# Optimization experiments

Hardware: AMD Instinct MI355X
Metric: run time of the kernel (lower is better)

Reference implementation:

```python
import jax, jax.numpy as jnp
import numpy as np

N_LAYER, N_HEAD, N_EMBD, VOCAB, T_CTX, MAXT, B = 6, 8, 128, 18, 30, 2719, 64


def _ln(x, g, b, eps=1e-5):
    m = x.mean(-1, keepdims=True)
    v = ((x - m) ** 2).mean(-1, keepdims=True)
    return (x - m) * jax.lax.rsqrt(v + eps) * g + b


def setup_inputs() -> dict:
    key = jax.random.key(0)
    ks = iter(jax.random.split(key, 64))
    nrm = lambda shape: jax.random.normal(next(ks), shape, jnp.float32) * 0.02
    E, L4 = N_EMBD, 4 * N_EMBD
    inp = dict(
        states=jax.random.normal(next(ks), (B, T_CTX, 4, 84, 84), jnp.float32),
        actions=jax.random.randint(next(ks), (B, T_CTX, 1), 0, VOCAB),
        rtgs=jax.random.normal(next(ks), (B, T_CTX, 1), jnp.float32),
        timesteps=jax.random.randint(next(ks), (B, 1, 1), 0, MAXT),
        conv_w=nrm((E, 4, 84, 84)),
        class_tok=nrm((1, 1, E)),
        in_proj_w=nrm((3 * E, E)), in_proj_b=jnp.zeros(3 * E),
        out_w=nrm((E, E)), out_b=jnp.zeros(E),
        iln1_g=jnp.ones(E), iln1_b=jnp.zeros(E),
        iln2_g=jnp.ones(E), iln2_b=jnp.zeros(E),
        ffn_w1=nrm((E, E)), ffn_b1=jnp.zeros(E),
        ffn_w2=nrm((E, E)), ffn_b2=jnp.zeros(E),
        ret_w=nrm((E, 1)), ret_b=jnp.zeros(E),
        act_table=nrm((VOCAB, E)),
        pos_emb=nrm((1, 3 * T_CTX + 1, E)),
        global_pos_emb=nrm((1, MAXT + 1, E)),
        ln1_g=jnp.ones((N_LAYER, E)), ln1_b=jnp.zeros((N_LAYER, E)),
        Wq=nrm((N_LAYER, E, E)), bq=jnp.zeros((N_LAYER, E)),
        Wk=nrm((N_LAYER, E, E)), bk=jnp.zeros((N_LAYER, E)),
        Wv=nrm((N_LAYER, E, E)), bv=jnp.zeros((N_LAYER, E)),
        Wo=nrm((N_LAYER, E, E)), bo=jnp.zeros((N_LAYER, E)),
        ln2_g=jnp.ones((N_LAYER, E)), ln2_b=jnp.zeros((N_LAYER, E)),
        W1=nrm((N_LAYER, L4, E)), b1=jnp.zeros((N_LAYER, L4)),
        W2=nrm((N_LAYER, E, L4)), b2=jnp.zeros((N_LAYER, E)),
        lnf_g=jnp.ones(E), lnf_b=jnp.zeros(E),
        head_w=nrm((VOCAB, E)),
    )
    return inp


def _forward(states, actions, rtgs, timesteps, conv_w, class_tok, in_proj_w, in_proj_b,
             out_w, out_b, iln1_g, iln1_b, iln2_g, iln2_b, ffn_w1, ffn_b1, ffn_w2, ffn_b2,
             ret_w, ret_b, act_table, pos_emb, global_pos_emb,
             ln1_g, ln1_b, Wq, bq, Wk, bk, Wv, bv, Wo, bo, ln2_g, ln2_b,
             W1, b1, W2, b2, lnf_g, lnf_b, head_w):
    Bsz, T = states.shape[:2]
    E = conv_w.shape[0]
    H, hd = N_HEAD, E // N_HEAD
    # --- inner TIT: patch embed (kernel 84 = frame size -> single patch = one big dot) ---
    obs = states.reshape(Bsz * T, *states.shape[2:])                      # (BT,4,84,84)
    patch = jnp.einsum('bchw,echw->be', obs, conv_w)[:, None, :]          # (BT,1,E)
    x = jnp.concatenate([jnp.broadcast_to(class_tok, (Bsz * T, 1, E)), patch], axis=1)  # (BT,2,E)
    h = _ln(x, iln1_g, iln1_b)
    q, k, v = jnp.split(h @ in_proj_w.T + in_proj_b, 3, axis=-1)
    att = jax.nn.softmax(jnp.einsum('bqe,bke->bqk', q, k) / jnp.sqrt(jnp.float32(E)), axis=-1)
    x = x + jnp.einsum('bqk,bke->bqe', att, v) @ out_w.T + out_b
    h2 = _ln(x, iln2_g, iln2_b)
    x = x + jax.nn.relu(h2 @ ffn_w1.T + ffn_b1) @ ffn_w2.T + ffn_b2
    state_emb = x[:, 0, :].reshape(Bsz, T, E)                             # class token
    # --- token interleave (targets=None path -> length 3T-1, last T-1 actions) ---
    rtg_emb = jnp.tanh(rtgs @ ret_w.T + ret_b)                            # (B,T,E)
    act_emb = jnp.tanh(act_table[actions[..., 0]])                        # (B,T,E)
    Lt = 3 * T - 1
    tok = jnp.zeros((Bsz, Lt, E), states.dtype)
    tok = tok.at[:, 0::3].set(rtg_emb).at[:, 1::3].set(state_emb).at[:, 2::3].set(act_emb[:, 1:])
    pos = global_pos_emb[0][timesteps[:, 0, 0]][:, None, :] + pos_emb[:, :Lt, :]
    x = tok + pos
    # --- outer causal GPT blocks ---
    mask = jnp.tril(jnp.ones((Lt, Lt), bool))
    for i in range(N_LAYER):
        hh = _ln(x, ln1_g[i], ln1_b[i])
        proj = lambda w, b: (hh @ w.T + b).reshape(Bsz, Lt, H, hd).transpose(0, 2, 1, 3)
        q, k, v = proj(Wq[i], bq[i]), proj(Wk[i], bk[i]), proj(Wv[i], bv[i])
        att = jnp.einsum('bhqd,bhkd->bhqk', q, k) / jnp.sqrt(jnp.float32(hd))
        att = jax.nn.softmax(jnp.where(mask, att, -jnp.inf), axis=-1)
        y = jnp.einsum('bhqk,bhkd->bhqd', att, v).transpose(0, 2, 1, 3).reshape(Bsz, Lt, E)
        x = x + y @ Wo[i].T + bo[i]
        hh2 = _ln(x, ln2_g[i], ln2_b[i])
        x = x + jax.nn.gelu(hh2 @ W1[i].T + b1[i], approximate=False) @ W2[i].T + b2[i]
    logits = _ln(x, lnf_g, lnf_b) @ head_w.T
    return logits[:, 1::3, :]                                             # (B,T,vocab) state-position logits


def reference(states, actions, rtgs, timesteps, conv_w, class_tok, in_proj_w, in_proj_b,
              out_w, out_b, iln1_g, iln1_b, iln2_g, iln2_b, ffn_w1, ffn_b1, ffn_w2, ffn_b2,
              ret_w, ret_b, act_table, pos_emb, global_pos_emb,
              ln1_g, ln1_b, Wq, bq, Wk, bk, Wv, bv, Wo, bo, ln2_g, ln2_b,
              W1, b1, W2, b2, lnf_g, lnf_b, head_w):
    return _forward(states, actions, rtgs, timesteps, conv_w, class_tok, in_proj_w, in_proj_b,
                    out_w, out_b, iln1_g, iln1_b, iln2_g, iln2_b, ffn_w1, ffn_b1, ffn_w2, ffn_b2,
                    ret_w, ret_b, act_table, pos_emb, global_pos_emb,
                    ln1_g, ln1_b, Wq, bq, Wk, bk, Wv, bv, Wo, bo, ln2_g, ln2_b,
                    W1, b1, W2, b2, lnf_g, lnf_b, head_w)
```

## Files before the change

### kernel.cpp

```cpp
#include <hip/hip_runtime.h>

#define NB   64
#define NT   30
#define NBT  1920
#define EE   128
#define KP   28224
#define LTK  89
#define NS   5696
#define NLY  6
#define NV   18
#define NZ   21

typedef unsigned short ushort_t;
using bf16x8 = __attribute__((ext_vector_type(8))) short;
using us8    = __attribute__((ext_vector_type(8))) unsigned short;
using f32x4  = __attribute__((ext_vector_type(4))) float;
using f32x16 = __attribute__((ext_vector_type(16))) float;

__device__ inline ushort_t f2bf(float f){
  union { float f; unsigned u; } v; v.f = f;
  unsigned r = v.u + 0x7FFFu + ((v.u >> 16) & 1u);
  return (ushort_t)(r >> 16);
}

__global__ __launch_bounds__(256) void wcvt(
  const float* conv, const float* Wq, const float* Wk, const float* Wv,
  const float* Wo, const float* W1, const float* W2,
  const float* in_w, const float* out_w, const float* f1w, const float* f2w,
  const float* bq, const float* bk, const float* bv,
  ushort_t* dc, ushort_t* dqkv, ushort_t* dout, ushort_t* d1, ushort_t* d2,
  ushort_t* dinw, ushort_t* doutw, ushort_t* df1, ushort_t* df2, float* bqkv)
{
  if (blockIdx.x >= 4776){
    int idx = (blockIdx.x-4776)*256 + threadIdx.x;
    if (idx < NLY*128){ int l=idx>>7, j=idx&127;
      bqkv[l*384+j]=bq[idx]; bqkv[l*384+128+j]=bk[idx]; bqkv[l*384+256+j]=bv[idx]; }
    return;
  }
  long i = 4l*((long)blockIdx.x*256 + threadIdx.x);
  if (i >= 3612672l && i < 3907584l){
    long o = i - 3612672l;
    int  seg = (int)(o / 98304l);
    long off2 = o - (long)seg*98304l;
    long layer = off2 >> 14, rem = off2 & 16383l;
    const float* s = (seg==0) ? Wq : (seg==1) ? Wk : Wv;
    float4 f = *reinterpret_cast<const float4*>(s+off2);
    long dst = layer*49152l + (long)seg*16384l + rem;
    dqkv[dst]=f2bf(f.x); dqkv[dst+1]=f2bf(f.y); dqkv[dst+2]=f2bf(f.z); dqkv[dst+3]=f2bf(f.w);
    return;
  }
  const float* s; ushort_t* d; long off;
  if      (i < 3612672l){ s=conv;  d=dc;    off=i; }
  else if (i < 4005888l){ s=Wo;    d=dout;  off=i-3907584l; }
  else if (i < 4399104l){ s=W1;    d=d1;    off=i-4005888l; }
  else if (i < 4792320l){ s=W2;    d=d2;    off=i-4399104l; }
  else if (i < 4841472l){ s=in_w;  d=dinw;  off=i-4792320l; }
  else if (i < 4857856l){ s=out_w; d=doutw; off=i-4841472l; }
  else if (i < 4874240l){ s=f1w;   d=df1;   off=i-4857856l; }
  else                  { s=f2w;   d=df2;   off=i-4874240l; }
  float4 f = *reinterpret_cast<const float4*>(s+off);
  d[off]=f2bf(f.x); d[off+1]=f2bf(f.y); d[off+2]=f2bf(f.z); d[off+3]=f2bf(f.w);
}

__global__ __launch_bounds__(256) void patch_gemm(
  const float* __restrict__ A, const ushort_t* __restrict__ Wb, float* __restrict__ C)
{
  __shared__ __align__(16) ushort_t As[64*64];
  __shared__ __align__(16) ushort_t Ws[128*64];
  const int tid = threadIdx.x, lane = tid & 63, wid = tid >> 6;
  const int m0 = blockIdx.x * 64;
  const int kbase = blockIdx.z * 1344;
  float* Cz = C + (size_t)blockIdx.z * NBT * EE;
  const int ra = tid>>2, ca = (tid&3)*16, swa = (ra&7)<<3;
  const int rw = tid>>1, cw = (tid&1)*32, sww = (rw&7)<<3;
  const float*    Ab = A  + (size_t)(m0+ra)*KP + kbase + ca;
  const ushort_t* Wp = Wb + (size_t)rw*KP  + kbase + cw;
  f32x4 acc[8];
  #pragma unroll
  for (int j=0;j<8;j++) acc[j] = (f32x4){0.f,0.f,0.f,0.f};
  float4 fa[4]; us8 wr[4];
  #pragma unroll
  for (int q=0;q<4;q++) fa[q] = *reinterpret_cast<const float4*>(Ab + 4*q);
  #pragma unroll
  for (int q=0;q<4;q++) wr[q] = *reinterpret_cast<const us8*>(Wp + 8*q);

  for (int kt = 0; kt < 21; ++kt){
    { us8 o0, o1;
      o0[0]=f2bf(fa[0].x); o0[1]=f2bf(fa[0].y); o0[2]=f2bf(fa[0].z); o0[3]=f2bf(fa[0].w);
      o0[4]=f2bf(fa[1].x); o0[5]=f2bf(fa[1].y); o0[6]=f2bf(fa[1].z); o0[7]=f2bf(fa[1].w);
      o1[0]=f2bf(fa[2].x); o1[1]=f2bf(fa[2].y); o1[2]=f2bf(fa[2].z); o1[3]=f2bf(fa[2].w);
      o1[4]=f2bf(fa[3].x); o1[5]=f2bf(fa[3].y); o1[6]=f2bf(fa[3].z); o1[7]=f2bf(fa[3].w);
      *reinterpret_cast<us8*>(&As[ra*64 + ( ca    ^ swa)]) = o0;
      *reinterpret_cast<us8*>(&As[ra*64 + ((ca+8) ^ swa)]) = o1;
      #pragma unroll
      for (int q=0;q<4;q++)
        *reinterpret_cast<us8*>(&Ws[rw*64 + ((cw+8*q) ^ sww)]) = wr[q];
    }
    if (kt < 20){
      #pragma unroll
      for (int q=0;q<4;q++) fa[q] = *reinterpret_cast<const float4*>(Ab + (kt+1)*64 + 4*q);
      #pragma unroll
      for (int q=0;q<4;q++) wr[q] = *reinterpret_cast<const us8*>(Wp + (kt+1)*64 + 8*q);
    }
    __syncthreads();
    #pragma unroll
    for (int ks=0; ks<2; ++ks){
      int arow = wid*16 + (lane&15);
      int kb = ks*32 + (lane>>4)*8;
      bf16x8 a = *reinterpret_cast<const bf16x8*>(&As[arow*64 + (kb ^ ((arow&7)<<3))]);
      #pragma unroll
      for (int nt=0; nt<8; ++nt){
        int nn = nt*16 + (lane&15);
        bf16x8 b = *reinterpret_cast<const bf16x8*>(&Ws[nn*64 + (kb ^ ((nn&7)<<3))]);
        acc[nt] = __builtin_amdgcn_mfma_f32_16x16x32_bf16(a, b, acc[nt], 0,0,0);
      }
    }
    __syncthreads();
  }
  #pragma unroll
  for (int nt=0; nt<8; ++nt)
    #pragma unroll
    for (int rr=0;rr<4;rr++){
      int row = m0 + wid*16 + (lane>>4)*4 + rr;
      int col = nt*16 + (lane&15);
      Cz[row*EE + col] = acc[nt][rr];
    }
}

__global__ __launch_bounds__(256, 1) void inner_tit(
  const float* __restrict__ part, const float* __restrict__ ctok,
  const ushort_t* __restrict__ inw, const float* __restrict__ in_b,
  const ushort_t* __restrict__ outw, const float* __restrict__ out_b,
  const float* __restrict__ g1, const float* __restrict__ b1_,
  const float* __restrict__ g2, const float* __restrict__ b2_,
  const ushort_t* __restrict__ f1wb, const float* __restrict__ fb1,
  const ushort_t* __restrict__ f2wb, const float* __restrict__ fb2,
  const float* __restrict__ rtgs, const int* __restrict__ actions,
  const int* __restrict__ tsteps, const float* __restrict__ ret_w,
  const float* __restrict__ ret_b, const float* __restrict__ act_tab,
  const float* __restrict__ pos_emb, const float* __restrict__ gpos,
  const float* __restrict__ ln1g0, const float* __restrict__ ln1b0,
  float* __restrict__ x, ushort_t* __restrict__ xln)
{
  __shared__ __align__(16) ushort_t wbuf[384*128];
  __shared__ float xs[16*128];
  __shared__ __align__(16) ushort_t hb[16*128];
  __shared__ __align__(16) ushort_t hf[16*128];
  __shared__ float qkv[16*384];
  __shared__ float ssm[32];
  const int tid = threadIdx.x, lane = tid & 63, wid = tid >> 6;
  const int bt0 = blockIdx.x * 8;

  auto stageWB = [&](const ushort_t* src, int R, int rowoff){
    for (int c = tid; c < R*16; c += 256){
      int rr = c >> 4, cc = (c & 15) * 8;
      *reinterpret_cast<us8*>(&wbuf[(rowoff+rr)*128 + (cc ^ ((rr&7)<<3))]) =
        *reinterpret_cast<const us8*>(src + (size_t)rr*128 + cc);
    }
  };
  auto lnrow = [&](const float* gam, const float* bet, ushort_t* dst){
    int r = tid >> 4, e0 = (tid & 15) * 8;
    float v[8];
    #pragma unroll
    for (int j=0;j<8;j++) v[j] = xs[r*128 + e0 + j];
    float s = 0;
    #pragma unroll
    for (int j=0;j<8;j++) s += v[j];
    s += __shfl_xor(s,1); s += __shfl_xor(s,2); s += __shfl_xor(s,4); s += __shfl_xor(s,8);
    float mean = s * (1.0f/128.0f);
    float vs = 0;
    #pragma unroll
    for (int j=0;j<8;j++){ float d = v[j]-mean; vs += d*d; }
    vs += __shfl_xor(vs,1); vs += __shfl_xor(vs,2); vs += __shfl_xor(vs,4); vs += __shfl_xor(vs,8);
    float rstd = rsqrtf(vs*(1.0f/128.0f) + 1e-5f);
    us8 o;
    #pragma unroll
    for (int j=0;j<8;j++) o[j] = f2bf((v[j]-mean)*rstd*gam[e0+j] + bet[e0+j]);
    *reinterpret_cast<us8*>(&dst[r*128 + (e0 ^ ((r&7)<<3))]) = o;
  };

  { int r = tid >> 4, e0 = (tid & 15) * 8;
    float v[8];
    if ((r & 1) == 0){
      #pragma unroll
      for (int j=0;j<8;j++) v[j] = ctok[e0+j];
    } else {
      #pragma unroll
      for (int j=0;j<8;j++) v[j] = 0.f;
      int bt = bt0 + (r>>1);
      for (int z=0; z<NZ; ++z){
        const float* p = part + (size_t)z*NBT*EE + (size_t)bt*128 + e0;
        float4 f0 = *reinterpret_cast<const float4*>(p);
        float4 f1 = *reinterpret_cast<const float4*>(p+4);
        v[0]+=f0.x; v[1]+=f0.y; v[2]+=f0.z; v[3]+=f0.w;
        v[4]+=f1.x; v[5]+=f1.y; v[6]+=f1.z; v[7]+=f1.w;
      }
    }
    #pragma unroll
    for (int j=0;j<8;j++) xs[r*128 + e0 + j] = v[j];
  }
  stageWB(inw, 384, 0);
  __syncthreads();

  lnrow(g1, b1_, hb);
  __syncthreads();

  { int al = lane & 15, kq = (lane>>4)*8;
    #pragma unroll
    for (int j=0;j<6;++j){
      int nt = wid*6 + j;
      f32x4 acc = (f32x4){0.f,0.f,0.f,0.f};
      int nrow = nt*16 + al, nsw = (nrow&7)<<3;
      #pragma unroll
      for (int ks=0; ks<4; ++ks){
        int kb = ks*32 + kq;
        bf16x8 a = *reinterpret_cast<const bf16x8*>(&hb[al*128 + (kb ^ ((al&7)<<3))]);
        bf16x8 b = *reinterpret_cast<const bf16x8*>(&wbuf[nrow*128 + (kb ^ nsw)]);
        acc = __builtin_amdgcn_mfma_f32_16x16x32_bf16(a, b, acc, 0,0,0);
      }
      float bia = in_b[nt*16 + al];
      #pragma unroll
      for (int rr=0; rr<4; ++rr){
        int row = (lane>>4)*4 + rr;
        qkv[row*384 + nt*16 + al] = acc[rr] + bia;
      }
    }
  }
  __syncthreads();

  { int d = tid >> 3, j = tid & 7;
    int i = d >> 2, p = d & 3;
    const float* qp = &qkv[(2*i + (p>>1))*384 + j*16];
    const float* kp = &qkv[(2*i + (p&1))*384 + 128 + j*16];
    float s = 0;
    #pragma unroll
    for (int e=0;e<16;e++) s += qp[e]*kp[e];
    s += __shfl_xor(s,1); s += __shfl_xor(s,2); s += __shfl_xor(s,4);
    if (j == 0) ssm[d] = s;
  }
  stageWB(outw, 128, 0);
  stageWB(f1wb, 128, 128);
  stageWB(f2wb, 128, 256);
  __syncthreads();

  { int r = tid >> 4, e0 = (tid & 15)*8;
    int i = r >> 1, t = r & 1;
    const float sc = 0.08838834764831845f;
    float s0 = ssm[i*4 + t*2]*sc, s1 = ssm[i*4 + t*2 + 1]*sc;
    float m = fmaxf(s0,s1), p0 = __expf(s0-m), p1 = __expf(s1-m);
    float iv = 1.0f/(p0+p1); p0 *= iv; p1 *= iv;
    const float* v0 = &qkv[(2*i)*384 + 256 + e0];
    const float* v1 = &qkv[(2*i+1)*384 + 256 + e0];
    us8 o;
    #pragma unroll
    for (int j=0;j<8;j++) o[j] = f2bf(p0*v0[j] + p1*v1[j]);
    *reinterpret_cast<us8*>(&hb[r*128 + (e0 ^ ((r&7)<<3))]) = o;
  }
  __syncthreads();

  { int al = lane & 15, kq = (lane>>4)*8;
    #pragma unroll
    for (int j=0;j<2;++j){
      int nt = wid*2 + j;
      f32x4 acc = (f32x4){0.f,0.f,0.f,0.f};
      int nrow = nt*16 + al, nsw = (nrow&7)<<3;
      #pragma unroll
      for (int ks=0; ks<4; ++ks){
        int kb = ks*32 + kq;
        bf16x8 a = *reinterpret_cast<const bf16x8*>(&hb[al*128 + (kb ^ ((al&7)<<3))]);
        bf16x8 b = *reinterpret_cast<const bf16x8*>(&wbuf[nrow*128 + (kb ^ nsw)]);
        acc = __builtin_amdgcn_mfma_f32_16x16x32_bf16(a, b, acc, 0,0,0);
      }
      float bia = out_b[nt*16 + al];
      #pragma unroll
      for (int rr=0; rr<4; ++rr){
        int row = (lane>>4)*4 + rr;
        xs[row*128 + nt*16 + al] += acc[rr] + bia;
      }
    }
  }
  __syncthreads();

  lnrow(g2, b2_, hb);
  __syncthreads();

  { int al = lane & 15, kq = (lane>>4)*8;
    #pragma unroll
    for (int j=0;j<2;++j){
      int nt = wid*2 + j;
      f32x4 acc = (f32x4){0.f,0.f,0.f,0.f};
      int nrow = nt*16 + al, nsw = (nrow&7)<<3;
      #pragma unroll
      for (int ks=0; ks<4; ++ks){
        int kb = ks*32 + kq;
        bf16x8 a = *reinterpret_cast<const bf16x8*>(&hb[al*128 + (kb ^ ((al&7)<<3))]);
        bf16x8 b = *reinterpret_cast<const bf16x8*>(&wbuf[(128+nrow)*128 + (kb ^ nsw)]);
        acc = __builtin_amdgcn_mfma_f32_16x16x32_bf16(a, b, acc, 0,0,0);
      }
      float bia = fb1[nt*16 + al];
      #pragma unroll
      for (int rr=0; rr<4; ++rr){
        int row = (lane>>4)*4 + rr;
        hf[row*128 + ((nt*16+al) ^ ((row&7)<<3))] = f2bf(fmaxf(acc[rr] + bia, 0.f));
      }
    }
  }
  __syncthreads();

  { int al = lane & 15, kq = (lane>>4)*8;
    #pragma unroll
    for (int j=0;j<2;++j){
      int nt = wid*2 + j;
      f32x4 acc = (f32x4){0.f,0.f,0.f,0.f};
      int nrow = nt*16 + al, nsw = (nrow&7)<<3;
      #pragma unroll
      for (int ks=0; ks<4; ++ks){
        int kb = ks*32 + kq;
        bf16x8 a = *reinterpret_cast<const bf16x8*>(&hf[al*128 + (kb ^ ((al&7)<<3))]);
        bf16x8 b = *reinterpret_cast<const bf16x8*>(&wbuf[(256+nrow)*128 + (kb ^ nsw)]);
        acc = __builtin_amdgcn_mfma_f32_16x16x32_bf16(a, b, acc, 0,0,0);
      }
      float bia = fb2[nt*16 + al];
      #pragma unroll
      for (int rr=0; rr<4; ++rr){
        int row = (lane>>4)*4 + rr;
        xs[row*128 + nt*16 + al] += acc[rr] + bia;
      }
    }
  }
  __syncthreads();

  { int q = tid >> 3, j = tid & 7;
    if (q < 24){
      int i = q / 3, kind = q - 3*i;
      int btg = bt0 + i, b = btg / NT, t = btg - b*NT;
      bool valid = !(kind == 2 && t == 0);
      if (valid){
        int prow = (kind==0) ? 3*t : (kind==1) ? 3*t+1 : 3*t-1;
        size_t xrow = ((size_t)b*LTK + prow)*128;
        int ts = tsteps[b];
        int e0 = j*16;
        float v[16];
        if (kind == 1){
          #pragma unroll
          for (int e=0;e<16;e++) v[e] = xs[(2*i)*128 + e0 + e];
        } else if (kind == 0){
          float rv = rtgs[b*NT+t];
          #pragma unroll
          for (int e=0;e<16;e++) v[e] = tanhf(rv*ret_w[e0+e] + ret_b[e0+e]);
        } else {
          int a = actions[b*NT+t];
          #pragma unroll
          for (int e=0;e<16;e++) v[e] = tanhf(act_tab[a*128 + e0 + e]);
        }
        #pragma unroll
        for (int e=0;e<16;e++)
          v[e] += gpos[(size_t)ts*128 + e0 + e] + pos_emb[prow*128 + e0 + e];
        #pragma unroll
        for (int e=0;e<16;e++) x[xrow + e0 + e] = v[e];
        float s = 0;
        #pragma unroll
        for (int e=0;e<16;e++) s += v[e];
        s += __shfl_xor(s,1); s += __shfl_xor(s,2); s += __shfl_xor(s,4);
        float mean = s * (1.0f/128.0f);
        float vs = 0;
        #pragma unroll
        for (int e=0;e<16;e++){ float d = v[e]-mean; vs += d*d; }
        vs += __shfl_xor(vs,1); vs += __shfl_xor(vs,2); vs += __shfl_xor(vs,4);
        float rstd = rsqrtf(vs*(1.0f/128.0f) + 1e-5f);
        #pragma unroll
        for (int e=0;e<16;e++)
          xln[xrow + e0 + e] = f2bf((v[e]-mean)*rstd*ln1g0[e0+e] + ln1b0[e0+e]);
      }
    }
  }
}

template<bool HEAD>
__global__ __launch_bounds__(256, 2) void layer_fused(
  const ushort_t* __restrict__ xln, float* __restrict__ x,
  const ushort_t* __restrict__ Wqkv, const float* __restrict__ bqkv,
  const ushort_t* __restrict__ Wo, const float* __restrict__ bo,
  const float* __restrict__ g2, const float* __restrict__ b2g,
  const ushort_t* __restrict__ W1, const float* __restrict__ b1v,
  const ushort_t* __restrict__ W2, const float* __restrict__ b2v,
  const float* __restrict__ lnng, const float* __restrict__ lnnb,
  ushort_t* __restrict__ xlnout,
  const float* __restrict__ lnfg, const float* __restrict__ lnfb,
  const float* __restrict__ hw, float* __restrict__ out)
{
  __shared__ __align__(16) char sm[73088];
  ushort_t* kln = (ushort_t*)sm;
  ushort_t* wb  = (ushort_t*)(sm + 24576);
  ushort_t* qa  = (ushort_t*)(sm + 36864);
  ushort_t* ka  = (ushort_t*)(sm + 38272);
  ushort_t* vta = (ushort_t*)(sm + 42496);
  float*    S   = (float*)(sm + 45824);
  ushort_t* pb  = (ushort_t*)(sm + 58112);
  float*    inv = (float*)(sm + 64768);
  ushort_t* yb  = (ushort_t*)(sm + 64896);
  ushort_t* wdb = (ushort_t*)sm;
  float*    xr  = (float*)(sm + 32768);
  ushort_t* h2  = (ushort_t*)(sm + 49664);
  ushort_t* f1  = (ushort_t*)(sm + 64896);

  const int tid = threadIdx.x, lane = tid & 63, wid = tid >> 6;
  const int b = blockIdx.x / 3, j = blockIdx.x % 3;
  const int R0 = j*32;
  const int P  = (j==2) ? LTK : R0 + 32;
  const int SR = R0 + 32;
  const int PT16 = (P+15)>>4, PT32 = (P+31)>>5;
  const int VR = (j==2) ? (LTK-64) : 32;
  const int m0g = b*LTK + R0;

  for (int idx = tid; idx < SR*16; idx += 256){
    int row = idx >> 4, c0 = (idx & 15)*8;
    us8 v;
    if (row < LTK) v = *reinterpret_cast<const us8*>(xln + ((size_t)(b*LTK+row))*128 + c0);
    else           v = (us8){0,0,0,0,0,0,0,0};
    *reinterpret_cast<us8*>(&kln[row*128 + (c0 ^ ((row&7)<<3))]) = v;
  }
  __syncthreads();

  for (int h = 0; h < 8; ++h){
    for (int idx = tid; idx < 384; idx += 256){
      int rr = idx >> 3, c = (idx & 7)*16;
      int seg = rr >> 4, n = rr & 15;
      const ushort_t* src = Wqkv + (size_t)(seg*128 + h*16 + n)*128 + c;
      int sw = (rr&7)<<3;
      *reinterpret_cast<us8*>(&wb[rr*128 + ( c    ^ sw)]) = *reinterpret_cast<const us8*>(src);
      *reinterpret_cast<us8*>(&wb[rr*128 + ((c+8) ^ sw)]) = *reinterpret_cast<const us8*>(src+8);
    }
    __syncthreads();
    { int NU = 2 + 2*PT16;
      for (int u = wid; u < NU; u += 4){
        int typ, rt;
        if (u < 2)            { typ = 0; rt = u; }
        else if (u < 2+PT16)  { typ = 1; rt = u-2; }
        else                  { typ = 2; rt = u-2-PT16; }
        int al = lane & 15;
        int arow = ((typ==0)? R0 : 0) + rt*16 + al;
        int asw = (arow&7)<<3;
        int nrow = typ*16 + al, nsw = (nrow&7)<<3;
        f32x4 acc = (f32x4){0.f,0.f,0.f,0.f};
        #pragma unroll
        for (int ks=0; ks<4; ++ks){
          int kb = ks*32 + (lane>>4)*8;
          bf16x8 a  = *reinterpret_cast<const bf16x8*>(&kln[arow*128 + (kb ^ asw)]);
          bf16x8 bf = *reinterpret_cast<const bf16x8*>(&wb[nrow*128 + (kb ^ nsw)]);
          acc = __builtin_amdgcn_mfma_f32_16x16x32_bf16(a, bf, acc, 0,0,0);
        }
        float bia = bqkv[typ*128 + h*16 + al];
        #pragma unroll
        for (int rr=0; rr<4; ++rr){
          int rg = rt*16 + (lane>>4)*4 + rr;
          ushort_t hv = f2bf(acc[rr] + bia);
          if      (typ == 0) qa[rg*22 + al] = hv;
          else if (typ == 1) ka[rg*22 + al] = hv;
          else               vta[al*104 + rg] = hv;
        }
      }
    }
    __syncthreads();
    for (int ct = wid; ct < PT32; ct += 4){
      int ke = (lane>>5)*8;
      bf16x8 a  = *reinterpret_cast<const bf16x8*>(&qa[(lane&31)*22 + ke]);
      bf16x8 bf = *reinterpret_cast<const bf16x8*>(&ka[(ct*32+(lane&31))*22 + ke]);
      f32x16 sc = {};
      sc = __builtin_amdgcn_mfma_f32_32x32x16_bf16(a, bf, sc, 0,0,0);
      #pragma unroll
      for (int r=0; r<16; ++r){
        int rin = (r&3) + 8*(r>>2) + 4*(lane>>5);
        S[rin*96 + ct*32 + (lane&31)] = sc[r]*0.25f;
      }
    }
    __syncthreads();
    { int r = tid >> 3, q8 = tid & 7;
      int tg = R0 + r, u0 = q8*12, lim = PT32*32;
      float sv[12];
      float mx = -1e30f;
      #pragma unroll
      for (int k=0;k<12;k++){
        int u = u0+k;
        float s = (u < lim && u <= tg) ? S[r*96+u] : -1e30f;
        sv[k] = s; mx = fmaxf(mx, s);
      }
      mx = fmaxf(mx, __shfl_xor(mx,1));
      mx = fmaxf(mx, __shfl_xor(mx,2));
      mx = fmaxf(mx, __shfl_xor(mx,4));
      float sum = 0;
      #pragma unroll
      for (int k=0;k<12;k++){
        float p = (sv[k] > -1e29f) ? __expf(sv[k]-mx) : 0.f;
        sum += p;
        pb[r*104 + u0 + k] = f2bf(p);
      }
      sum += __shfl_xor(sum,1); sum += __shfl_xor(sum,2); sum += __shfl_xor(sum,4);
      if (q8 == 0) inv[r] = 1.0f/sum;
    }
    __syncthreads();
    for (int rt = wid; rt < 2; rt += 4){
      int arow = rt*16 + (lane&15);
      f32x4 acc = (f32x4){0.f,0.f,0.f,0.f};
      for (int ks=0; ks<PT32; ++ks){
        int kb = ks*32 + (lane>>4)*8;
        bf16x8 a  = *reinterpret_cast<const bf16x8*>(&pb[arow*104 + kb]);
        bf16x8 bf = *reinterpret_cast<const bf16x8*>(&vta[(lane&15)*104 + kb]);
        acc = __builtin_amdgcn_mfma_f32_16x16x32_bf16(a, bf, acc, 0,0,0);
      }
      #pragma unroll
      for (int rr=0; rr<4; ++rr){
        int row = rt*16 + (lane>>4)*4 + rr;
        yb[row*128 + ((h*16+(lane&15)) ^ ((row&7)<<3))] = f2bf(acc[rr]*inv[row]);
      }
    }
    __syncthreads();
  }

  auto stageW = [&](const ushort_t* src_base, size_t stride, int buf){
    int rr = tid >> 2, q = tid & 3, sw = (rr&7)<<3;
    const ushort_t* s = src_base + (size_t)rr*stride + q*32;
    ushort_t* d = wdb + buf*8192 + rr*128;
    #pragma unroll
    for (int g=0; g<4; ++g)
      *reinterpret_cast<us8*>(&d[(q*32+g*8) ^ sw]) =
        *reinterpret_cast<const us8*>(s + g*8);
  };
  auto gemmT = [&](const ushort_t* abuf, int buf, f32x4* accp){
    int nrow = wid*16 + (lane&15), nsw = (nrow&7)<<3;
    const ushort_t* wbp = wdb + buf*8192;
    #pragma unroll
    for (int rt=0; rt<2; ++rt){
      int arow = rt*16 + (lane&15), asw = (arow&7)<<3;
      #pragma unroll
      for (int ks=0; ks<4; ++ks){
        int kb = ks*32 + (lane>>4)*8;
        bf16x8 a  = *reinterpret_cast<const bf16x8*>(&abuf[arow*128 + (kb ^ asw)]);
        bf16x8 bb = *reinterpret_cast<const bf16x8*>(&wbp[nrow*128 + (kb ^ nsw)]);
        accp[rt] = __builtin_amdgcn_mfma_f32_16x16x32_bf16(a, bb, accp[rt], 0,0,0);
      }
    }
  };

  stageW(Wo, 128, 0);
  __syncthreads();
  f32x4 accA[2][2];
  #pragma unroll
  for (int s_=0;s_<2;++s_){ accA[s_][0]=(f32x4){0,0,0,0}; accA[s_][1]=(f32x4){0,0,0,0}; }
  stageW(Wo + 64*128, 128, 1);
  gemmT(yb, 0, accA[0]);
  __syncthreads();
  gemmT(yb, 1, accA[1]);
  #pragma unroll
  for (int s_=0; s_<2; ++s_){
    int col = s_*64 + wid*16 + (lane&15);
    float bia = bo[col];
    #pragma unroll
    for (int rt=0; rt<2; ++rt)
      #pragma unroll
      for (int rr=0; rr<4; ++rr){
        int row = rt*16 + (lane>>4)*4 + rr;
        float xv_in = (row < VR) ? x[(size_t)(m0g+row)*128 + col] : 0.f;
        xr[row*132 + col] = accA[s_][rt][rr] + bia + xv_in;
      }
  }
  __syncthreads();

  { int r = tid>>3, q = tid&7;
    float xv[16];
    #pragma unroll
    for (int i=0;i<16;i++) xv[i] = xr[r*132 + q*16 + i];
    float s = 0;
    #pragma unroll
    for (int i=0;i<16;i++) s += xv[i];
    s += __shfl_xor(s,1); s += __shfl_xor(s,2); s += __shfl_xor(s,4);
    float mean = s * (1.0f/128.0f);
    float vs = 0;
    #pragma unroll
    for (int i=0;i<16;i++){ float d = xv[i]-mean; vs += d*d; }
    vs += __shfl_xor(vs,1); vs += __shfl_xor(vs,2); vs += __shfl_xor(vs,4);
    float rstd = rsqrtf(vs*(1.0f/128.0f) + 1e-5f);
    int sw = (r&7)<<3;
    #pragma unroll
    for (int g=0; g<2; ++g){
      us8 o;
      #pragma unroll
      for (int jj=0;jj<8;jj++){
        int c = q*16 + g*8 + jj;
        o[jj] = f2bf((xv[g*8+jj]-mean)*rstd*g2[c] + b2g[c]);
      }
      *reinterpret_cast<us8*>(&h2[r*128 + ((q*16+g*8) ^ sw)]) = o;
    }
  }
  stageW(W1, 128, 0);
  __syncthreads();

  f32x4 acc2[2][2];
  #pragma unroll
  for (int s_=0;s_<2;++s_){ acc2[s_][0]=(f32x4){0,0,0,0}; acc2[s_][1]=(f32x4){0,0,0,0}; }
  int buf = 0;
  for (int c=0; c<4; ++c){
    stageW(W1 + (size_t)(c*128+64)*128, 128, buf^1);
    { f32x4 ac[2] = {(f32x4){0,0,0,0},(f32x4){0,0,0,0}};
      gemmT(h2, buf, ac);
      int cl = wid*16 + (lane&15);
      float bia = b1v[c*128 + cl];
      #pragma unroll
      for (int rt=0; rt<2; ++rt)
        #pragma unroll
        for (int rr=0; rr<4; ++rr){
          int row = rt*16 + (lane>>4)*4 + rr;
          float v = ac[rt][rr] + bia;
          v = 0.5f*v*(1.0f + erff(v*0.70710678118654752f));
          f1[row*128 + (cl ^ ((row&7)<<3))] = f2bf(v);
        }
    }
    __syncthreads();
    stageW(W2 + (size_t)c*128, 512, buf);
    { f32x4 ac[2] = {(f32x4){0,0,0,0},(f32x4){0,0,0,0}};
      gemmT(h2, buf^1, ac);
      int cl = 64 + wid*16 + (lane&15);
      float bia = b1v[c*128 + cl];
      #pragma unroll
      for (int rt=0; rt<2; ++rt)
        #pragma unroll
        for (int rr=0; rr<4; ++rr){
          int row = rt*16 + (lane>>4)*4 + rr;
          float v = ac[rt][rr] + bia;
          v = 0.5f*v*(1.0f + erff(v*0.70710678118654752f));
          f1[row*128 + (cl ^ ((row&7)<<3))] = f2bf(v);
        }
    }
    __syncthreads();
    stageW(W2 + (size_t)64*512 + (size_t)c*128, 512, buf^1);
    gemmT(f1, buf, acc2[0]);
    __syncthreads();
    if (c < 3) stageW(W1 + (size_t)((c+1)*128)*128, 128, buf);
    gemmT(f1, buf^1, acc2[1]);
    __syncthreads();
  }

  #pragma unroll
  for (int s_=0; s_<2; ++s_){
    int col = s_*64 + wid*16 + (lane&15);
    float bia = b2v[col];
    #pragma unroll
    for (int rt=0; rt<2; ++rt)
      #pragma unroll
      for (int rr=0; rr<4; ++rr){
        int row = rt*16 + (lane>>4)*4 + rr;
        float v = acc2[s_][rt][rr] + bia + xr[row*132 + col];
        xr[row*132 + col] = v;
        if constexpr (!HEAD){
          if (row < VR) x[(size_t)(m0g+row)*128 + col] = v;
        }
      }
  }
  __syncthreads();
  if constexpr (!HEAD){
    int r = tid>>3, q = tid&7;
    if (r < VR){
      float xv[16];
      #pragma unroll
      for (int i=0;i<16;i++) xv[i] = xr[r*132 + q*16 + i];
      float s = 0;
      #pragma unroll
      for (int i=0;i<16;i++) s += xv[i];
      s += __shfl_xor(s,1); s += __shfl_xor(s,2); s += __shfl_xor(s,4);
      float mean = s * (1.0f/128.0f);
      float vs = 0;
      #pragma unroll
      for (int i=0;i<16;i++){ float d = xv[i]-mean; vs += d*d; }
      vs += __shfl_xor(vs,1); vs += __shfl_xor(vs,2); vs += __shfl_xor(vs,4);
      float rstd = rsqrtf(vs*(1.0f/128.0f) + 1e-5f);
      #pragma unroll
      for (int g=0; g<2; ++g){
        us8 o;
        #pragma unroll
        for (int jj=0;jj<8;jj++){
          int c = q*16 + g*8 + jj;
          o[jj] = f2bf((xv[g*8+jj]-mean)*rstd*lnng[c] + lnnb[c]);
        }
        *reinterpret_cast<us8*>(xlnout + (size_t)(m0g+r)*128 + q*16 + g*8) = o;
      }
    }
  } else {
    for (int r = wid; r < VR; r += 4){
      int s = m0g + r, bb2 = s / LTK, p = s - bb2*LTK;
      if (p % 3 != 1) continue;
      int t = p / 3;
      float v1 = xr[r*132 + lane];
      float v2 = xr[r*132 + 64 + lane];
      float sum = v1 + v2;
      sum += __shfl_xor(sum,1); sum += __shfl_xor(sum,2); sum += __shfl_xor(sum,4);
      sum += __shfl_xor(sum,8); sum += __shfl_xor(sum,16); sum += __shfl_xor(sum,32);
      float mean = sum*(1.0f/128.0f);
      float d1 = v1-mean, d2 = v2-mean;
      float var = d1*d1 + d2*d2;
      var += __shfl_xor(var,1); var += __shfl_xor(var,2); var += __shfl_xor(var,4);
      var += __shfl_xor(var,8); var += __shfl_xor(var,16); var += __shfl_xor(var,32);
      float rstd = rsqrtf(var*(1.0f/128.0f) + 1e-5f);
      float h1 = d1*rstd*lnfg[lane]    + lnfb[lane];
      float h2v= d2*rstd*lnfg[lane+64] + lnfb[lane+64];
      #pragma unroll
      for (int o=0; o<NV; ++o){
        float sdot = h1*hw[o*128+lane] + h2v*hw[o*128+lane+64];
        sdot += __shfl_xor(sdot,1); sdot += __shfl_xor(sdot,2); sdot += __shfl_xor(sdot,4);
        sdot += __shfl_xor(sdot,8); sdot += __shfl_xor(sdot,16); sdot += __shfl_xor(sdot,32);
        if (lane == 0) out[(size_t)(bb2*NT+t)*NV + o] = sdot;
      }
    }
  }
}

extern "C" void kernel_launch(void* const* d_in, const int* in_sizes, int n_in,
                              void* d_out, int out_size, void* d_ws, size_t ws_size,
                              hipStream_t stream)
{
  const float* states  = (const float*)d_in[0];
  const int*   actions = (const int*)  d_in[1];
  const float* rtgs    = (const float*)d_in[2];
  const int*   tsteps  = (const int*)  d_in[3];
  const float* conv_w  = (const float*)d_in[4];
  const float* ctok    = (const float*)d_in[5];
  const float* in_w    = (const float*)d_in[6];
  const float* in_b    = (const float*)d_in[7];
  const float* out_w   = (const float*)d_in[8];
  const float* out_b   = (const float*)d_in[9];
  const float* i1g     = (const float*)d_in[10];
  const float* i1b     = (const float*)d_in[11];
  const float* i2g     = (const float*)d_in[12];
  const float* i2b     = (const float*)d_in[13];
  const float* fw1     = (const float*)d_in[14];
  const float* fb1     = (const float*)d_in[15];
  const float* fw2     = (const float*)d_in[16];
  const float* fb2     = (const float*)d_in[17];
  const float* ret_w   = (const float*)d_in[18];
  const float* ret_b   = (const float*)d_in[19];
  const float* act_tab = (const float*)d_in[20];
  const float* pos_emb = (const float*)d_in[21];
  const float* gpos    = (const float*)d_in[22];
  const float* ln1g    = (const float*)d_in[23];
  const float* ln1b    = (const float*)d_in[24];
  const float* Wq      = (const float*)d_in[25];
  const float* bq      = (const float*)d_in[26];
  const float* Wk      = (const float*)d_in[27];
  const float* bk      = (const float*)d_in[28];
  const float* Wv      = (const float*)d_in[29];
  const float* bv      = (const float*)d_in[30];
  const float* Wo      = (const float*)d_in[31];
  const float* bo      = (const float*)d_in[32];
  const float* ln2g    = (const float*)d_in[33];
  const float* ln2b    = (const float*)d_in[34];
  const float* W1      = (const float*)d_in[35];
  const float* b1      = (const float*)d_in[36];
  const float* W2      = (const float*)d_in[37];
  const float* b2      = (const float*)d_in[38];
  const float* lnfg    = (const float*)d_in[39];
  const float* lnfb    = (const float*)d_in[40];
  const float* head_w  = (const float*)d_in[41];

  char* w = (char*)d_ws;
  size_t off = 0;
  auto alloc = [&](size_t bytes)->char* {
    char* p = w + off; off += (bytes + 255) & ~(size_t)255; return p;
  };
  float*    part  = (float*)   alloc((size_t)NZ*NBT*EE*4);
  float*    x     = (float*)   alloc((size_t)NS*EE*4);
  ushort_t* xlnA  = (ushort_t*)alloc((size_t)NS*EE*2);
  ushort_t* xlnB  = (ushort_t*)alloc((size_t)NS*EE*2);
  ushort_t* cwb   = (ushort_t*)alloc((size_t)EE*KP*2);
  ushort_t* Wqkvb = (ushort_t*)alloc((size_t)NLY*384*128*2);
  ushort_t* Wob   = (ushort_t*)alloc((size_t)NLY*128*128*2);
  ushort_t* W1b   = (ushort_t*)alloc((size_t)NLY*512*128*2);
  ushort_t* W2b   = (ushort_t*)alloc((size_t)NLY*128*512*2);
  ushort_t* inwb  = (ushort_t*)alloc((size_t)384*128*2);
  ushort_t* outwb = (ushort_t*)alloc((size_t)128*128*2);
  ushort_t* f1wb  = (ushort_t*)alloc((size_t)128*128*2);
  ushort_t* f2wb  = (ushort_t*)alloc((size_t)128*128*2);
  float*    bqkv  = (float*)   alloc(NLY*384*4);
  (void)in_sizes; (void)n_in; (void)out_size; (void)ws_size;

  wcvt<<<4779,256,0,stream>>>(conv_w,Wq,Wk,Wv,Wo,W1,W2,
                              in_w,out_w,fw1,fw2, bq,bk,bv,
                              cwb,Wqkvb,Wob,W1b,W2b,
                              inwb,outwb,f1wb,f2wb, bqkv);
  patch_gemm<<<dim3(30,1,NZ),256,0,stream>>>(states, cwb, part);
  inner_tit<<<240,256,0,stream>>>(part, ctok, inwb, in_b, outwb, out_b,
                                  i1g,i1b,i2g,i2b, f1wb,fb1, f2wb,fb2,
                                  rtgs, actions, tsteps, ret_w, ret_b, act_tab,
                                  pos_emb, gpos, ln1g, ln1b, x, xlnA);
  for (int i=0;i<NLY;i++){
    ushort_t* xin  = (i & 1) ? xlnB : xlnA;
    ushort_t* xout = (i & 1) ? xlnA : xlnB;
    if (i < NLY-1)
      layer_fused<false><<<192,256,0,stream>>>(
        xin, x, Wqkvb+(size_t)i*49152, bqkv+(size_t)i*384,
        Wob+(size_t)i*16384, bo+i*128, ln2g+i*128, ln2b+i*128,
        W1b+(size_t)i*65536, b1+i*512, W2b+(size_t)i*65536, b2+i*128,
        ln1g+(i+1)*128, ln1b+(i+1)*128, xout,
        nullptr, nullptr, nullptr, nullptr);
    else
      layer_fused<true><<<192,256,0,stream>>>(
        xin, x, Wqkvb+(size_t)i*49152, bqkv+(size_t)i*384,
        Wob+(size_t)i*16384, bo+i*128, ln2g+i*128, ln2b+i*128,
        W1b+(size_t)i*65536, b1+i*512, W2b+(size_t)i*65536, b2+i*128,
        nullptr, nullptr, nullptr,
        lnfg, lnfb, head_w, (float*)d_out);
  }
}
```

Measured before the change: 393.0 us.

## Compute full QKV projection once, then process attention two heads per pass

The QKV projection now runs as three full 128-wide segment GEMMs, one each for Q, K and V, and the results are kept in a much larger shared-memory buffer. This replaces the eight per-head projections and their weight staging. Attention then handles two heads per iteration, so the number of barrier-separated phases drops and each phase has more parallel work for the four waves. The cost is about 122 KB of LDS and a launch bound of one block per CU instead of two, which lowers occupancy.

```diff
diff --git a/kernel.cpp b/kernel.cpp
--- a/kernel.cpp
+++ b/kernel.cpp
@@ -377,7 +377,7 @@
 }
 
 template<bool HEAD>
-__global__ __launch_bounds__(256, 2) void layer_fused(
+__global__ __launch_bounds__(256, 1) void layer_fused(
   const ushort_t* __restrict__ xln, float* __restrict__ x,
   const ushort_t* __restrict__ Wqkv, const float* __restrict__ bqkv,
   const ushort_t* __restrict__ Wo, const float* __restrict__ bo,
@@ -389,20 +389,20 @@
   const float* __restrict__ lnfg, const float* __restrict__ lnfb,
   const float* __restrict__ hw, float* __restrict__ out)
 {
-  __shared__ __align__(16) char sm[73088];
-  ushort_t* kln = (ushort_t*)sm;
-  ushort_t* wb  = (ushort_t*)(sm + 24576);
-  ushort_t* qa  = (ushort_t*)(sm + 36864);
-  ushort_t* ka  = (ushort_t*)(sm + 38272);
-  ushort_t* vta = (ushort_t*)(sm + 42496);
-  float*    S   = (float*)(sm + 45824);
-  ushort_t* pb  = (ushort_t*)(sm + 58112);
-  float*    inv = (float*)(sm + 64768);
-  ushort_t* yb  = (ushort_t*)(sm + 64896);
-  ushort_t* wdb = (ushort_t*)sm;
-  float*    xr  = (float*)(sm + 32768);
-  ushort_t* h2  = (ushort_t*)(sm + 49664);
-  ushort_t* f1  = (ushort_t*)(sm + 64896);
+  __shared__ __align__(16) char sm[124928];
+  ushort_t* xlnS = (ushort_t*)sm;
+  ushort_t* wqs  = (ushort_t*)(sm + 24576);
+  float*    S    = (float*)sm;
+  ushort_t* pb   = (ushort_t*)(sm + 25600);
+  float*    inv  = (float*)(sm + 38912);
+  ushort_t* qa   = (ushort_t*)(sm + 57344);
+  ushort_t* ka   = (ushort_t*)(sm + 65536);
+  ushort_t* vta  = (ushort_t*)(sm + 90112);
+  ushort_t* yb   = (ushort_t*)(sm + 116736);
+  ushort_t* wdb  = (ushort_t*)sm;
+  float*    xr   = (float*)(sm + 32768);
+  ushort_t* h2   = (ushort_t*)(sm + 49664);
+  ushort_t* f1   = (ushort_t*)(sm + 57856);
 
   const int tid = threadIdx.x, lane = tid & 63, wid = tid >> 6;
   const int b = blockIdx.x / 3, j = blockIdx.x % 3;
@@ -418,100 +418,105 @@
     us8 v;
     if (row < LTK) v = *reinterpret_cast<const us8*>(xln + ((size_t)(b*LTK+row))*128 + c0);
     else           v = (us8){0,0,0,0,0,0,0,0};
-    *reinterpret_cast<us8*>(&kln[row*128 + (c0 ^ ((row&7)<<3))]) = v;
-  }
-  __syncthreads();
-
-  for (int h = 0; h < 8; ++h){
-    for (int idx = tid; idx < 384; idx += 256){
-      int rr = idx >> 3, c = (idx & 7)*16;
-      int seg = rr >> 4, n = rr & 15;
-      const ushort_t* src = Wqkv + (size_t)(seg*128 + h*16 + n)*128 + c;
+    *reinterpret_cast<us8*>(&xlnS[row*128 + (c0 ^ ((row&7)<<3))]) = v;
+  }
+  __syncthreads();
+
+  for (int seg = 0; seg < 3; ++seg){
+    for (int idx = tid; idx < 1024; idx += 256){
+      int rr = idx >> 3, c = (idx & 7) * 16;
+      const ushort_t* src = Wqkv + (size_t)(seg*128 + rr)*128 + c;
       int sw = (rr&7)<<3;
-      *reinterpret_cast<us8*>(&wb[rr*128 + ( c    ^ sw)]) = *reinterpret_cast<const us8*>(src);
-      *reinterpret_cast<us8*>(&wb[rr*128 + ((c+8) ^ sw)]) = *reinterpret_cast<const us8*>(src+8);
-    }
-    __syncthreads();
-    { int NU = 2 + 2*PT16;
-      for (int u = wid; u < NU; u += 4){
-        int typ, rt;
-        if (u < 2)            { typ = 0; rt = u; }
-        else if (u < 2+PT16)  { typ = 1; rt = u-2; }
-        else                  { typ = 2; rt = u-2-PT16; }
-        int al = lane & 15;
-        int arow = ((typ==0)? R0 : 0) + rt*16 + al;
-        int asw = (arow&7)<<3;
-        int nrow = typ*16 + al, nsw = (nrow&7)<<3;
-        f32x4 acc = (f32x4){0.f,0.f,0.f,0.f};
-        #pragma unroll
-        for (int ks=0; ks<4; ++ks){
-          int kb = ks*32 + (lane>>4)*8;
-          bf16x8 a  = *reinterpret_cast<const bf16x8*>(&kln[arow*128 + (kb ^ asw)]);
-          bf16x8 bf = *reinterpret_cast<const bf16x8*>(&wb[nrow*128 + (kb ^ nsw)]);
-          acc = __builtin_amdgcn_mfma_f32_16x16x32_bf16(a, bf, acc, 0,0,0);
-        }
-        float bia = bqkv[typ*128 + h*16 + al];
-        #pragma unroll
-        for (int rr=0; rr<4; ++rr){
-          int rg = rt*16 + (lane>>4)*4 + rr;
-          ushort_t hv = f2bf(acc[rr] + bia);
-          if      (typ == 0) qa[rg*22 + al] = hv;
-          else if (typ == 1) ka[rg*22 + al] = hv;
-          else               vta[al*104 + rg] = hv;
-        }
-      }
-    }
-    __syncthreads();
-    for (int ct = wid; ct < PT32; ct += 4){
-      int ke = (lane>>5)*8;
-      bf16x8 a  = *reinterpret_cast<const bf16x8*>(&qa[(lane&31)*22 + ke]);
-      bf16x8 bf = *reinterpret_cast<const bf16x8*>(&ka[(ct*32+(lane&31))*22 + ke]);
+      *reinterpret_cast<us8*>(&wqs[rr*128 + ( c    ^ sw)]) = *reinterpret_cast<const us8*>(src);
+      *reinterpret_cast<us8*>(&wqs[rr*128 + ((c+8) ^ sw)]) = *reinterpret_cast<const us8*>(src+8);
+    }
+    __syncthreads();
+    int NU = (seg==0) ? 16 : PT16*8;
+    for (int u = wid; u < NU; u += 4){
+      int rt = u >> 3, nt = u & 7;
+      int al = lane & 15;
+      int arow = ((seg==0)? R0 : 0) + rt*16 + al;
+      int asw = (arow&7)<<3;
+      int nrow = nt*16 + al, nsw = (nrow&7)<<3;
+      f32x4 acc = (f32x4){0.f,0.f,0.f,0.f};
+      #pragma unroll
+      for (int ks=0; ks<4; ++ks){
+        int kb = ks*32 + (lane>>4)*8;
+        bf16x8 a  = *reinterpret_cast<const bf16x8*>(&xlnS[arow*128 + (kb ^ asw)]);
+        bf16x8 bf = *reinterpret_cast<const bf16x8*>(&wqs[nrow*128 + (kb ^ nsw)]);
+        acc = __builtin_amdgcn_mfma_f32_16x16x32_bf16(a, bf, acc, 0,0,0);
+      }
+      float bia = bqkv[seg*128 + nt*16 + al];
+      #pragma unroll
+      for (int rr=0; rr<4; ++rr){
+        int rg = rt*16 + (lane>>4)*4 + rr;
+        ushort_t hv = f2bf(acc[rr] + bia);
+        int col = nt*16 + al;
+        if      (seg == 0) qa[rg*128 + (col ^ ((rg&7)<<3))] = hv;
+        else if (seg == 1) ka[rg*128 + (col ^ ((rg&7)<<3))] = hv;
+        else               vta[col*104 + rg] = hv;
+      }
+    }
+    __syncthreads();
+  }
+
+  const int lim = PT32*32;
+  for (int hp = 0; hp < 4; ++hp){
+    for (int u = wid; u < 2*PT32; u += 4){
+      int hh = u / PT32, ct = u - hh*PT32;
+      int h = hp*2 + hh;
+      int ar = lane & 31;
+      int ke = h*16 + (lane>>5)*8;
+      bf16x8 a  = *reinterpret_cast<const bf16x8*>(&qa[ar*128 + (ke ^ ((ar&7)<<3))]);
+      int br = ct*32 + (lane&31);
+      bf16x8 bf = *reinterpret_cast<const bf16x8*>(&ka[br*128 + (ke ^ ((br&7)<<3))]);
       f32x16 sc = {};
       sc = __builtin_amdgcn_mfma_f32_32x32x16_bf16(a, bf, sc, 0,0,0);
       #pragma unroll
       for (int r=0; r<16; ++r){
         int rin = (r&3) + 8*(r>>2) + 4*(lane>>5);
-        S[rin*96 + ct*32 + (lane&31)] = sc[r]*0.25f;
-      }
-    }
-    __syncthreads();
-    { int r = tid >> 3, q8 = tid & 7;
-      int tg = R0 + r, u0 = q8*12, lim = PT32*32;
-      float sv[12];
+        S[hh*3200 + rin*100 + ct*32 + (lane&31)] = sc[r]*0.25f;
+      }
+    }
+    __syncthreads();
+    { int r6 = tid >> 2, q4 = tid & 3;
+      int hh = r6 >> 5, r = r6 & 31;
+      int tg = R0 + r, u0 = q4*24;
+      float sv[24];
       float mx = -1e30f;
       #pragma unroll
-      for (int k=0;k<12;k++){
+      for (int k=0;k<24;k++){
         int u = u0+k;
-        float s = (u < lim && u <= tg) ? S[r*96+u] : -1e30f;
+        float s = (u < lim && u <= tg) ? S[hh*3200 + r*100 + u] : -1e30f;
         sv[k] = s; mx = fmaxf(mx, s);
       }
       mx = fmaxf(mx, __shfl_xor(mx,1));
       mx = fmaxf(mx, __shfl_xor(mx,2));
-      mx = fmaxf(mx, __shfl_xor(mx,4));
       float sum = 0;
       #pragma unroll
-      for (int k=0;k<12;k++){
+      for (int k=0;k<24;k++){
         float p = (sv[k] > -1e29f) ? __expf(sv[k]-mx) : 0.f;
         sum += p;
-        pb[r*104 + u0 + k] = f2bf(p);
-      }
-      sum += __shfl_xor(sum,1); sum += __shfl_xor(sum,2); sum += __shfl_xor(sum,4);
-      if (q8 == 0) inv[r] = 1.0f/sum;
-    }
-    __syncthreads();
-    for (int rt = wid; rt < 2; rt += 4){
+        pb[hh*3328 + r*104 + u0 + k] = f2bf(p);
+      }
+      sum += __shfl_xor(sum,1); sum += __shfl_xor(sum,2);
+      if (q4 == 0) inv[hh*32+r] = 1.0f/sum;
+    }
+    __syncthreads();
+    { int u = wid;
+      int hh = u >> 1, rt = u & 1, h = hp*2 + hh;
       int arow = rt*16 + (lane&15);
       f32x4 acc = (f32x4){0.f,0.f,0.f,0.f};
       for (int ks=0; ks<PT32; ++ks){
         int kb = ks*32 + (lane>>4)*8;
-        bf16x8 a  = *reinterpret_cast<const bf16x8*>(&pb[arow*104 + kb]);
-        bf16x8 bf = *reinterpret_cast<const bf16x8*>(&vta[(lane&15)*104 + kb]);
+        bf16x8 a  = *reinterpret_cast<const bf16x8*>(&pb[hh*3328 + arow*104 + kb]);
+        bf16x8 bf = *reinterpret_cast<const bf16x8*>(&vta[(h*16+(lane&15))*104 + kb]);
         acc = __builtin_amdgcn_mfma_f32_16x16x32_bf16(a, bf, acc, 0,0,0);
       }
       #pragma unroll
       for (int rr=0; rr<4; ++rr){
         int row = rt*16 + (lane>>4)*4 + rr;
-        yb[row*128 + ((h*16+(lane&15)) ^ ((row&7)<<3))] = f2bf(acc[rr]*inv[row]);
+        yb[row*128 + ((h*16+(lane&15)) ^ ((row&7)<<3))] = f2bf(acc[rr]*inv[hh*32+row]);
       }
     }
     __syncthreads();
```

Result: faster. 365.9 us (-6.9%).
